# Kernel tuning notes

Measured on AMD Instinct MI355X. Metric: run time of the kernel, lower is better.

The kernel has to match this reference:

```python
import jax, jax.numpy as jnp
import numpy as np
from itertools import product

GRID = 256          # voxels per axis
SCALE = 0.005       # regular grid spacing (transform diagonal)
OFFSET = -0.64      # grid origin (transform translation)
K = 2_000_000       # number of query points


def setup_inputs() -> dict:
    key = jax.random.key(0)
    kx, kv = jax.random.split(key)
    # query points uniform in [-0.6, 0.6]^3 (inside grid domain)
    x = (jax.random.uniform(kx, (K, 3), dtype=jnp.float32) - 0.5) * 1.2
    # SDF voxel grid values
    values = jax.random.normal(kv, (GRID, GRID, GRID), dtype=jnp.float32)
    # regular per-axis grid point coordinates (as in get_grid_pts)
    ax = (jnp.arange(GRID, dtype=jnp.float32) * SCALE + OFFSET)
    return {"x": x, "values": values, "px": ax, "py": ax, "pz": ax}


def _trilinear_interp(pts_xyz, values, axes):
    # pts_xyz: [K,3]; values: [Nx,Ny,Nz]; axes: (px,py,pz) sorted 1D coords
    idxs, dists, overalls = [], [], []
    for d, p in enumerate(axes):
        c = pts_xyz[:, d]                               # [K]
        n = p.shape[0]
        # torch.bucketize(x, p) with right=False == searchsorted side='left'
        ir = jnp.searchsorted(p, c, side="left")
        ir = jnp.minimum(ir, n - 1)
        il = jnp.clip(ir - 1, 0, n - 1)
        dl = jnp.maximum(c - p[il], 0.0)
        dr = jnp.maximum(p[ir] - c, 0.0)
        both_zero = (dl == 0.0) & (dr == 0.0)           # exactly on a grid point
        dl = jnp.where(both_zero, 1.0, dl)
        dr = jnp.where(both_zero, 1.0, dr)
        idxs.append((il, ir))
        dists.append((dl, dr))
        overalls.append(dl + dr)
    numerator = 0.0
    for onoff in product([0, 1], repeat=3):             # 8 corners
        ix, iy, iz = (idx[o] for o, idx in zip(onoff, idxs))
        w = dists[0][1 - onoff[0]] * dists[1][1 - onoff[1]] * dists[2][1 - onoff[2]]
        numerator = numerator + values[ix, iy, iz] * w
    denominator = overalls[0] * overalls[1] * overalls[2]
    return numerator / denominator                      # [K]


def reference(x, values, px, py, pz):
    pts = x.reshape(-1, 3).astype(jnp.float32)
    return _trilinear_interp(pts, values, (px, py, pz))  # squeezed [K]
```

## Files before the change

### kernel.cpp

```cpp
#include <hip/hip_runtime.h>

#define GRIDN 256
#define BPA 8
#define NBINS (BPA * BPA * BPA)
#define CAP 6144
#define CURSOR_STRIDE 16
#define FKEYS 512


__device__ __forceinline__ int cell_guess(float c) {
    float t = (c + 0.64f) * 200.0f;
    int i = (int)t;
    return min(max(i, 0), GRIDN - 1);
}

__device__ __forceinline__ void dim_interp(float c, const float* __restrict__ p,
                                           int& il, int& ir, float& dl, float& dr) {
    const float SCALE = 0.005f;
    const float OFFSET = -0.64f;
    float t = (c - OFFSET) * (1.0f / SCALE);
    int i = (int)ceilf(t);
    i = min(max(i, 0), GRIDN - 1);
    while (i < GRIDN - 1 && p[i] < c) ++i;
    while (i > 0 && p[i - 1] >= c) --i;
    ir = i;
    il = max(i - 1, 0);
    dl = fmaxf(c - p[il], 0.0f);
    dr = fmaxf(p[ir] - c, 0.0f);
    if (dl == 0.0f && dr == 0.0f) { dl = 1.0f; dr = 1.0f; }
}

__device__ __forceinline__ float interp_point_ax(float cx, float cy, float cz,
                                                 const float* __restrict__ values,
                                                 const float* __restrict__ ax,
                                                 const float* __restrict__ ay,
                                                 const float* __restrict__ az) {
    int ixl, ixr, iyl, iyr, izl, izr;
    float dxl, dxr, dyl, dyr, dzl, dzr;
    dim_interp(cx, ax, ixl, ixr, dxl, dxr);
    dim_interp(cy, ay, iyl, iyr, dyl, dyr);
    dim_interp(cz, az, izl, izr, dzl, dzr);
    int bxl = ixl << 16, bxr = ixr << 16;
    int byl = iyl << 8,  byr = iyr << 8;
    float num =
        values[bxl + byl + izl] * (dxr * dyr * dzr) +
        values[bxl + byl + izr] * (dxr * dyr * dzl) +
        values[bxl + byr + izl] * (dxr * dyl * dzr) +
        values[bxl + byr + izr] * (dxr * dyl * dzl) +
        values[bxr + byl + izl] * (dxl * dyr * dzr) +
        values[bxr + byl + izr] * (dxl * dyr * dzl) +
        values[bxr + byr + izl] * (dxl * dyl * dzr) +
        values[bxr + byr + izr] * (dxl * dyl * dzl);
    float den = (dxl + dxr) * (dyl + dyr) * (dzl + dzr);
    return num / den;
}

__device__ __forceinline__ float interp_zpair(float cx, float cy, float cz,
                                              const float* __restrict__ values,
                                              const float* __restrict__ sax) {
    int ixl, ixr, iyl, iyr, izl, izr;
    float dxl, dxr, dyl, dyr, dzl, dzr;
    dim_interp(cx, sax,             ixl, ixr, dxl, dxr);
    dim_interp(cy, sax + GRIDN,     iyl, iyr, dyl, dyr);
    dim_interp(cz, sax + 2 * GRIDN, izl, izr, dzl, dzr);

    int bxl = ixl << 16, bxr = ixr << 16;
    int byl = iyl << 8,  byr = iyr << 8;

    float2 vll, vlr, vrl, vrr;
    __builtin_memcpy(&vll, &values[bxl + byl + izl], 8);
    __builtin_memcpy(&vlr, &values[bxl + byr + izl], 8);
    __builtin_memcpy(&vrl, &values[bxr + byl + izl], 8);
    __builtin_memcpy(&vrr, &values[bxr + byr + izl], 8);

    bool zsame = (izr == izl);
    float zll = vll.x, zlr = zsame ? vll.x : vll.y;
    float yll = vlr.x, ylr = zsame ? vlr.x : vlr.y;
    float xll = vrl.x, xlr = zsame ? vrl.x : vrl.y;
    float wll = vrr.x, wlr = zsame ? vrr.x : vrr.y;

    float num =
        (dxr * dyr) * (zll * dzr + zlr * dzl) +
        (dxr * dyl) * (yll * dzr + ylr * dzl) +
        (dxl * dyr) * (xll * dzr + xlr * dzl) +
        (dxl * dyl) * (wll * dzr + wlr * dzl);
    float den = (dxl + dxr) * (dyl + dyr) * (dzl + dzr);
    return num / den;
}


__global__ void init_cursors(unsigned* __restrict__ cursor) {
    int t = blockIdx.x * blockDim.x + threadIdx.x;
    if (t < NBINS) cursor[t * CURSOR_STRIDE] = (unsigned)(t * CAP);
}


__global__ __launch_bounds__(1024) void bin_scatter2(
        const float* __restrict__ x, int K,
        unsigned* __restrict__ cursor,
        float4* __restrict__ records,
        int* __restrict__ inv,
        const float* __restrict__ values,
        const float* __restrict__ px,
        const float* __restrict__ py,
        const float* __restrict__ pz,
        float* __restrict__ out) {
    __shared__ unsigned cnt[NBINS];
    __shared__ unsigned slotcur[NBINS];

    int base = blockIdx.x * 4096;
    int end = min(base + 4096, K);

    for (int t = threadIdx.x; t < NBINS; t += 1024) cnt[t] = 0;
    __syncthreads();

    for (int i = base + threadIdx.x; i < end; i += 1024) {
        int bx = cell_guess(x[3 * i]) >> 5;
        int by = cell_guess(x[3 * i + 1]) >> 5;
        int bz = cell_guess(x[3 * i + 2]) >> 5;
        atomicAdd(&cnt[(bx * BPA + by) * BPA + bz], 1u);
    }
    __syncthreads();

    for (int t = threadIdx.x; t < NBINS; t += 1024)
        slotcur[t] = cnt[t] ? atomicAdd(&cursor[t * CURSOR_STRIDE], cnt[t]) : 0u;
    __syncthreads();

    for (int i = base + threadIdx.x; i < end; i += 1024) {
        float cx = x[3 * i], cy = x[3 * i + 1], cz = x[3 * i + 2];
        int bx = cell_guess(cx) >> 5;
        int by = cell_guess(cy) >> 5;
        int bz = cell_guess(cz) >> 5;
        int b = (bx * BPA + by) * BPA + bz;
        unsigned s = atomicAdd(&slotcur[b], 1u);
        if (s < (unsigned)((b + 1) * CAP)) {
            records[s] = make_float4(cx, cy, cz, 0.0f);
            inv[i] = (int)s;
        } else {
            inv[i] = -1;
            out[i] = interp_point_ax(cx, cy, cz, values, px, py, pz);
        }
    }
}


#define K2_THREADS 1024

__global__ __launch_bounds__(K2_THREADS) void interp_binsort(
        const float4* __restrict__ records,
        const unsigned* __restrict__ cursor,
        const float* __restrict__ values,
        const float* __restrict__ px,
        const float* __restrict__ py,
        const float* __restrict__ pz,
        float* __restrict__ res) {
    __shared__ float sax[3 * GRIDN];
    __shared__ unsigned hist[FKEYS];
    __shared__ unsigned short skeys[CAP];
    __shared__ unsigned short order[CAP];
    __shared__ float sx[CAP], sy[CAP], sz[CAP];
    __shared__ float sres[CAP];

    int nb = gridDim.x;
    int b = blockIdx.x;
    int q = nb >> 3;
    int bin = (b & 7) * q + (b >> 3);

    for (int t = threadIdx.x; t < GRIDN; t += K2_THREADS) {
        sax[t] = px[t];
        sax[GRIDN + t] = py[t];
        sax[2 * GRIDN + t] = pz[t];
    }
    for (int t = threadIdx.x; t < FKEYS; t += K2_THREADS) hist[t] = 0;
    __syncthreads();

    unsigned binstart = (unsigned)bin * CAP;
    unsigned segend = min(cursor[bin * CURSOR_STRIDE], binstart + CAP);
    int npts = (int)(segend - binstart);
    if (npts <= 0) return;

    int cbx = (bin >> 6) << 5;
    int cby = ((bin >> 3) & 7) << 5;
    int cbz = (bin & 7) << 5;

    for (int pt = threadIdx.x; pt < npts; pt += K2_THREADS) {
        float4 rec = records[binstart + pt];
        sx[pt] = rec.x; sy[pt] = rec.y; sz[pt] = rec.z;
        int fx = (cell_guess(rec.x) - cbx) >> 2;
        int fy = (cell_guess(rec.y) - cby) >> 2;
        int fz = (cell_guess(rec.z) - cbz) >> 2;
        fx = min(max(fx, 0), 7); fy = min(max(fy, 0), 7); fz = min(max(fz, 0), 7);
        int k = ((fx << 3) | fy) << 3 | fz;
        skeys[pt] = (unsigned short)k;
        atomicAdd(&hist[k], 1u);
    }
    __syncthreads();

    unsigned own = (threadIdx.x < FKEYS) ? hist[threadIdx.x] : 0u;
    for (int off = 1; off < FKEYS; off <<= 1) {
        unsigned v = 0;
        if (threadIdx.x < FKEYS && (int)threadIdx.x >= off) v = hist[threadIdx.x - off];
        __syncthreads();
        if (threadIdx.x < FKEYS) hist[threadIdx.x] += v;
        __syncthreads();
    }
    if (threadIdx.x < FKEYS) hist[threadIdx.x] -= own;
    __syncthreads();

    for (int pt = threadIdx.x; pt < npts; pt += K2_THREADS) {
        unsigned slot = atomicAdd(&hist[skeys[pt]], 1u);
        order[slot] = (unsigned short)pt;
    }
    __syncthreads();

    for (int pt = threadIdx.x; pt < npts; pt += K2_THREADS) {
        int j = order[pt];
        sres[j] = interp_zpair(sx[j], sy[j], sz[j], values, sax);
    }
    __syncthreads();

    for (int pt = threadIdx.x; pt < npts; pt += K2_THREADS)
        res[binstart + pt] = sres[pt];
}


__global__ void unscatter(const int* __restrict__ inv,
                          const float* __restrict__ res,
                          float* __restrict__ out, int K) {
    int i = blockIdx.x * blockDim.x + threadIdx.x;
    if (i >= K) return;
    int s = inv[i];
    if (s >= 0) out[i] = res[s];
}


__global__ void trilerp_direct(const float* __restrict__ x,
                               const float* __restrict__ values,
                               const float* __restrict__ px,
                               const float* __restrict__ py,
                               const float* __restrict__ pz,
                               float* __restrict__ out, int K) {
    int i = blockIdx.x * blockDim.x + threadIdx.x;
    if (i >= K) return;
    out[i] = interp_point_ax(x[3 * i], x[3 * i + 1], x[3 * i + 2],
                             values, px, py, pz);
}

extern "C" void kernel_launch(void* const* d_in, const int* in_sizes, int n_in,
                              void* d_out, int out_size, void* d_ws, size_t ws_size,
                              hipStream_t stream) {
    const float* x      = (const float*)d_in[0];
    const float* values = (const float*)d_in[1];
    const float* px     = (const float*)d_in[2];
    const float* py     = (const float*)d_in[3];
    const float* pz     = (const float*)d_in[4];
    float* out = (float*)d_out;

    int K = in_sizes[0] / 3;

    size_t cursor_bytes  = (size_t)NBINS * CURSOR_STRIDE * 4;
    size_t records_bytes = (size_t)NBINS * CAP * 16;
    size_t inv_bytes     = (size_t)K * 4;
    size_t res_bytes     = (size_t)NBINS * CAP * 4;
    size_t need = cursor_bytes + records_bytes + inv_bytes + res_bytes;

    if (ws_size < need) {
        int grid = (K + 255) / 256;
        trilerp_direct<<<grid, 256, 0, stream>>>(x, values, px, py, pz, out, K);
        return;
    }

    char* p = (char*)d_ws;
    unsigned* cursor = (unsigned*)p;  p += cursor_bytes;
    float4* records  = (float4*)p;    p += records_bytes;
    int* inv         = (int*)p;       p += inv_bytes;
    float* res       = (float*)p;

    init_cursors<<<2, 256, 0, stream>>>(cursor);

    int nblk1 = (K + 4095) / 4096;
    bin_scatter2<<<nblk1, 1024, 0, stream>>>(x, K, cursor, records, inv,
                                             values, px, py, pz, out);

    interp_binsort<<<NBINS, K2_THREADS, 0, stream>>>(records, cursor,
                                                     values, px, py, pz, res);

    int nblk3 = (K + 255) / 256;
    unscatter<<<nblk3, 256, 0, stream>>>(inv, res, out, K);
}
```

Before: 85.63 us.

## Use 1024 smaller bins, wave-shuffle histogram scan, and memset cursor init

Splits the grid into 1024 spatial bins, halving the z extent of each, with half the per-bin capacity. This shrinks the per-block shared memory footprint so more interp blocks can be resident and the grid is more evenly loaded. The 512-entry Hillis-Steele histogram scan with many barriers becomes a 256-entry wave-shuffle scan plus a small cross-wave fixup. Cursors are now relative offsets zeroed with a memset instead of an init kernel. More bins raise the chance of overflow into the slow direct fallback path.

```diff
diff --git a/kernel.cpp b/kernel.cpp
--- a/kernel.cpp
+++ b/kernel.cpp
@@ -1,11 +1,10 @@
 #include <hip/hip_runtime.h>
 
 #define GRIDN 256
-#define BPA 8
-#define NBINS (BPA * BPA * BPA)
-#define CAP 6144
+#define NBINS 1024
+#define CAP 3072
 #define CURSOR_STRIDE 16
-#define FKEYS 512
+#define FKEYS 256
 
 
 __device__ __forceinline__ int cell_guess(float c) {
@@ -88,10 +87,8 @@
     return num / den;
 }
 
-
-__global__ void init_cursors(unsigned* __restrict__ cursor) {
-    int t = blockIdx.x * blockDim.x + threadIdx.x;
-    if (t < NBINS) cursor[t * CURSOR_STRIDE] = (unsigned)(t * CAP);
+__device__ __forceinline__ int bin_of_cells(int cgx, int cgy, int cgz) {
+    return ((cgx >> 5) << 7) | ((cgy >> 5) << 4) | (cgz >> 4);
 }
 
 
@@ -115,23 +112,21 @@
     __syncthreads();
 
     for (int i = base + threadIdx.x; i < end; i += 1024) {
-        int bx = cell_guess(x[3 * i]) >> 5;
-        int by = cell_guess(x[3 * i + 1]) >> 5;
-        int bz = cell_guess(x[3 * i + 2]) >> 5;
-        atomicAdd(&cnt[(bx * BPA + by) * BPA + bz], 1u);
+        int b = bin_of_cells(cell_guess(x[3 * i]), cell_guess(x[3 * i + 1]),
+                             cell_guess(x[3 * i + 2]));
+        atomicAdd(&cnt[b], 1u);
     }
     __syncthreads();
 
     for (int t = threadIdx.x; t < NBINS; t += 1024)
-        slotcur[t] = cnt[t] ? atomicAdd(&cursor[t * CURSOR_STRIDE], cnt[t]) : 0u;
+        slotcur[t] = cnt[t] ? ((unsigned)t * CAP +
+                               atomicAdd(&cursor[t * CURSOR_STRIDE], cnt[t]))
+                            : 0u;
     __syncthreads();
 
     for (int i = base + threadIdx.x; i < end; i += 1024) {
         float cx = x[3 * i], cy = x[3 * i + 1], cz = x[3 * i + 2];
-        int bx = cell_guess(cx) >> 5;
-        int by = cell_guess(cy) >> 5;
-        int bz = cell_guess(cz) >> 5;
-        int b = (bx * BPA + by) * BPA + bz;
+        int b = bin_of_cells(cell_guess(cx), cell_guess(cy), cell_guess(cz));
         unsigned s = atomicAdd(&slotcur[b], 1u);
         if (s < (unsigned)((b + 1) * CAP)) {
             records[s] = make_float4(cx, cy, cz, 0.0f);
@@ -156,7 +151,8 @@
         float* __restrict__ res) {
     __shared__ float sax[3 * GRIDN];
     __shared__ unsigned hist[FKEYS];
-    __shared__ unsigned short skeys[CAP];
+    __shared__ unsigned wsum[4];
+    __shared__ unsigned char skeys[CAP];
     __shared__ unsigned short order[CAP];
     __shared__ float sx[CAP], sy[CAP], sz[CAP];
     __shared__ float sres[CAP];
@@ -171,17 +167,16 @@
         sax[GRIDN + t] = py[t];
         sax[2 * GRIDN + t] = pz[t];
     }
-    for (int t = threadIdx.x; t < FKEYS; t += K2_THREADS) hist[t] = 0;
+    if (threadIdx.x < FKEYS) hist[threadIdx.x] = 0;
     __syncthreads();
 
     unsigned binstart = (unsigned)bin * CAP;
-    unsigned segend = min(cursor[bin * CURSOR_STRIDE], binstart + CAP);
-    int npts = (int)(segend - binstart);
+    int npts = min((int)cursor[bin * CURSOR_STRIDE], CAP);
     if (npts <= 0) return;
 
-    int cbx = (bin >> 6) << 5;
-    int cby = ((bin >> 3) & 7) << 5;
-    int cbz = (bin & 7) << 5;
+    int cbx = (bin >> 7) << 5;
+    int cby = ((bin >> 4) & 7) << 5;
+    int cbz = (bin & 15) << 4;
 
     for (int pt = threadIdx.x; pt < npts; pt += K2_THREADS) {
         float4 rec = records[binstart + pt];
@@ -189,22 +184,31 @@
         int fx = (cell_guess(rec.x) - cbx) >> 2;
         int fy = (cell_guess(rec.y) - cby) >> 2;
         int fz = (cell_guess(rec.z) - cbz) >> 2;
-        fx = min(max(fx, 0), 7); fy = min(max(fy, 0), 7); fz = min(max(fz, 0), 7);
-        int k = ((fx << 3) | fy) << 3 | fz;
-        skeys[pt] = (unsigned short)k;
+        fx = min(max(fx, 0), 7); fy = min(max(fy, 0), 7); fz = min(max(fz, 0), 3);
+        int k = (((fx << 3) | fy) << 2) | fz;
+        skeys[pt] = (unsigned char)k;
         atomicAdd(&hist[k], 1u);
     }
     __syncthreads();
 
-    unsigned own = (threadIdx.x < FKEYS) ? hist[threadIdx.x] : 0u;
-    for (int off = 1; off < FKEYS; off <<= 1) {
-        unsigned v = 0;
-        if (threadIdx.x < FKEYS && (int)threadIdx.x >= off) v = hist[threadIdx.x - off];
-        __syncthreads();
-        if (threadIdx.x < FKEYS) hist[threadIdx.x] += v;
-        __syncthreads();
-    }
-    if (threadIdx.x < FKEYS) hist[threadIdx.x] -= own;
+    unsigned v = 0, s = 0;
+    int lane = threadIdx.x & 63, w = threadIdx.x >> 6;
+    if (threadIdx.x < FKEYS) {
+        v = hist[threadIdx.x];
+        s = v;
+        for (int off = 1; off < 64; off <<= 1) {
+            unsigned t = __shfl_up(s, off, 64);
+            if (lane >= off) s += t;
+        }
+        if (lane == 63) wsum[w] = s;
+    }
+    __syncthreads();
+    if (threadIdx.x == 0) {
+        unsigned a = 0;
+        for (int i = 0; i < 4; ++i) { unsigned t = wsum[i]; wsum[i] = a; a += t; }
+    }
+    __syncthreads();
+    if (threadIdx.x < FKEYS) hist[threadIdx.x] = s - v + wsum[w];
     __syncthreads();
 
     for (int pt = threadIdx.x; pt < npts; pt += K2_THREADS) {
@@ -276,7 +280,7 @@
     int* inv         = (int*)p;       p += inv_bytes;
     float* res       = (float*)p;
 
-    init_cursors<<<2, 256, 0, stream>>>(cursor);
+    hipMemsetAsync(cursor, 0, cursor_bytes, stream);
 
     int nblk1 = (K + 4095) / 4096;
     bin_scatter2<<<nblk1, 1024, 0, stream>>>(x, K, cursor, records, inv,
```

Result: slower. 95.22 us (+11.2%).

## Split each spatial bin across two blocks and use wave-shuffle prefix scan

Applied to the files above, without the earlier changes.

The interpolation kernel now launches two blocks per spatial bin, each sorting and interpolating half of the bin's points. This halves per-block shared memory so more blocks can be resident, and it doubles the grid size. The 512-entry histogram prefix sum becomes a warp-shuffle scan plus a small cross-wave fixup, replacing the barrier-heavy Hillis-Steele loop. Cursors now hold relative counts, so they are zeroed with a memset instead of an init kernel. The trade-off is that each half sorts only locally, which may reduce cache locality across the two halves of a bin.

```diff
diff --git a/kernel.cpp b/kernel.cpp
--- a/kernel.cpp
+++ b/kernel.cpp
@@ -4,6 +4,8 @@
 #define BPA 8
 #define NBINS (BPA * BPA * BPA)
 #define CAP 6144
+#define HALF 2
+#define CAPH (CAP / HALF)
 #define CURSOR_STRIDE 16
 #define FKEYS 512
 
@@ -89,12 +91,6 @@
 }
 
 
-__global__ void init_cursors(unsigned* __restrict__ cursor) {
-    int t = blockIdx.x * blockDim.x + threadIdx.x;
-    if (t < NBINS) cursor[t * CURSOR_STRIDE] = (unsigned)(t * CAP);
-}
-
-
 __global__ __launch_bounds__(1024) void bin_scatter2(
         const float* __restrict__ x, int K,
         unsigned* __restrict__ cursor,
@@ -123,7 +119,9 @@
     __syncthreads();
 
     for (int t = threadIdx.x; t < NBINS; t += 1024)
-        slotcur[t] = cnt[t] ? atomicAdd(&cursor[t * CURSOR_STRIDE], cnt[t]) : 0u;
+        slotcur[t] = cnt[t] ? ((unsigned)t * CAP +
+                               atomicAdd(&cursor[t * CURSOR_STRIDE], cnt[t]))
+                            : 0u;
     __syncthreads();
 
     for (int i = base + threadIdx.x; i < end; i += 1024) {
@@ -146,7 +144,7 @@
 
 #define K2_THREADS 1024
 
-__global__ __launch_bounds__(K2_THREADS) void interp_binsort(
+__global__ __launch_bounds__(K2_THREADS) void interp_halfsort(
         const float4* __restrict__ records,
         const unsigned* __restrict__ cursor,
         const float* __restrict__ values,
@@ -156,15 +154,18 @@
         float* __restrict__ res) {
     __shared__ float sax[3 * GRIDN];
     __shared__ unsigned hist[FKEYS];
-    __shared__ unsigned short skeys[CAP];
-    __shared__ unsigned short order[CAP];
-    __shared__ float sx[CAP], sy[CAP], sz[CAP];
-    __shared__ float sres[CAP];
+    __shared__ unsigned wsum[8];
+    __shared__ unsigned short skeys[CAPH];
+    __shared__ unsigned short order[CAPH];
+    __shared__ float sx[CAPH], sy[CAPH], sz[CAPH];
+    __shared__ float sres[CAPH];
 
     int nb = gridDim.x;
     int b = blockIdx.x;
     int q = nb >> 3;
-    int bin = (b & 7) * q + (b >> 3);
+    int lin = (b & 7) * q + (b >> 3);
+    int bin = lin >> 1;
+    int half = lin & 1;
 
     for (int t = threadIdx.x; t < GRIDN; t += K2_THREADS) {
         sax[t] = px[t];
@@ -175,52 +176,66 @@
     __syncthreads();
 
     unsigned binstart = (unsigned)bin * CAP;
-    unsigned segend = min(cursor[bin * CURSOR_STRIDE], binstart + CAP);
-    int npts = (int)(segend - binstart);
+    int npts = min((int)cursor[bin * CURSOR_STRIDE], CAP);
     if (npts <= 0) return;
+
+    int cnt_h = (npts + HALF - 1) / HALF;
+    int lo = half * cnt_h;
+    int n = min(npts, lo + cnt_h) - lo;
+    if (n <= 0) return;
+    unsigned base = binstart + lo;
 
     int cbx = (bin >> 6) << 5;
     int cby = ((bin >> 3) & 7) << 5;
     int cbz = (bin & 7) << 5;
 
-    for (int pt = threadIdx.x; pt < npts; pt += K2_THREADS) {
-        float4 rec = records[binstart + pt];
+    for (int pt = threadIdx.x; pt < n; pt += K2_THREADS) {
+        float4 rec = records[base + pt];
         sx[pt] = rec.x; sy[pt] = rec.y; sz[pt] = rec.z;
         int fx = (cell_guess(rec.x) - cbx) >> 2;
         int fy = (cell_guess(rec.y) - cby) >> 2;
         int fz = (cell_guess(rec.z) - cbz) >> 2;
         fx = min(max(fx, 0), 7); fy = min(max(fy, 0), 7); fz = min(max(fz, 0), 7);
-        int k = ((fx << 3) | fy) << 3 | fz;
+        int k = (((fx << 3) | fy) << 3) | fz;
         skeys[pt] = (unsigned short)k;
         atomicAdd(&hist[k], 1u);
     }
     __syncthreads();
 
-    unsigned own = (threadIdx.x < FKEYS) ? hist[threadIdx.x] : 0u;
-    for (int off = 1; off < FKEYS; off <<= 1) {
-        unsigned v = 0;
-        if (threadIdx.x < FKEYS && (int)threadIdx.x >= off) v = hist[threadIdx.x - off];
-        __syncthreads();
-        if (threadIdx.x < FKEYS) hist[threadIdx.x] += v;
-        __syncthreads();
-    }
-    if (threadIdx.x < FKEYS) hist[threadIdx.x] -= own;
-    __syncthreads();
-
-    for (int pt = threadIdx.x; pt < npts; pt += K2_THREADS) {
+    unsigned v = 0, s = 0;
+    int lane = threadIdx.x & 63, w = threadIdx.x >> 6;
+    if (threadIdx.x < FKEYS) {
+        v = hist[threadIdx.x];
+        s = v;
+        for (int off = 1; off < 64; off <<= 1) {
+            unsigned t = __shfl_up(s, off, 64);
+            if (lane >= off) s += t;
+        }
+        if (lane == 63) wsum[w] = s;
+    }
+    __syncthreads();
+    if (threadIdx.x == 0) {
+        unsigned a = 0;
+        for (int i = 0; i < 8; ++i) { unsigned t = wsum[i]; wsum[i] = a; a += t; }
+    }
+    __syncthreads();
+    if (threadIdx.x < FKEYS) hist[threadIdx.x] = s - v + wsum[w];
+    __syncthreads();
+
+    for (int pt = threadIdx.x; pt < n; pt += K2_THREADS) {
         unsigned slot = atomicAdd(&hist[skeys[pt]], 1u);
         order[slot] = (unsigned short)pt;
     }
     __syncthreads();
 
-    for (int pt = threadIdx.x; pt < npts; pt += K2_THREADS) {
+    for (int pt = threadIdx.x; pt < n; pt += K2_THREADS) {
         int j = order[pt];
         sres[j] = interp_zpair(sx[j], sy[j], sz[j], values, sax);
     }
     __syncthreads();
 
-    for (int pt = threadIdx.x; pt < npts; pt += K2_THREADS)
-        res[binstart + pt] = sres[pt];
+    for (int pt = threadIdx.x; pt < n; pt += K2_THREADS)
+        res[base + pt] = sres[pt];
 }
 
 
@@ -276,14 +291,14 @@
     int* inv         = (int*)p;       p += inv_bytes;
     float* res       = (float*)p;
 
-    init_cursors<<<2, 256, 0, stream>>>(cursor);
+    hipMemsetAsync(cursor, 0, cursor_bytes, stream);
 
     int nblk1 = (K + 4095) / 4096;
     bin_scatter2<<<nblk1, 1024, 0, stream>>>(x, K, cursor, records, inv,
                                              values, px, py, pz, out);
 
-    interp_binsort<<<NBINS, K2_THREADS, 0, stream>>>(records, cursor,
-                                                     values, px, py, pz, res);
+    interp_halfsort<<<NBINS * HALF, K2_THREADS, 0, stream>>>(records, cursor,
+                                                             values, px, py, pz, res);
 
     int nblk3 = (K + 255) / 256;
     unscatter<<<nblk3, 256, 0, stream>>>(inv, res, out, K);
```

Measured after the change: 82.37 us (median of 2 runs). 1.04x faster.

## Stage per-bin voxel region in shared memory instead of locally sorting points

Applied to the files above, without the earlier changes.

The per-bin interpolation kernel no longer sorts points with a shared-memory histogram. It now loads each bin's grid subregion (35x35x24 with a halo, in two z passes) into LDS and gathers the corner values from there, falling back to global gathers for points outside the staged region. Each thread keeps up to six point records in registers. The cursor is now zeroed with hipMemsetAsync and becomes a relative count, with the bin base added in the scatter kernel. This trades random global gathers for bulk coalesced tile loads, but each bin reloads a larger halo'd region and the kernel adds extra barriers.

```diff
diff --git a/kernel.cpp b/kernel.cpp
--- a/kernel.cpp
+++ b/kernel.cpp
@@ -5,7 +5,13 @@
 #define NBINS (BPA * BPA * BPA)
 #define CAP 6144
 #define CURSOR_STRIDE 16
-#define FKEYS 512
+#define RX 35
+#define RY 35
+#define RZ 24
+#define SEGS (RZ / 4)
+#define NROWS (RX * RY)
+#define REGF (NROWS * RZ)
+#define PPT 6
 
 
 __device__ __forceinline__ int cell_guess(float c) {
@@ -55,45 +61,6 @@
     return num / den;
 }
 
-__device__ __forceinline__ float interp_zpair(float cx, float cy, float cz,
-                                              const float* __restrict__ values,
-                                              const float* __restrict__ sax) {
-    int ixl, ixr, iyl, iyr, izl, izr;
-    float dxl, dxr, dyl, dyr, dzl, dzr;
-    dim_interp(cx, sax,             ixl, ixr, dxl, dxr);
-    dim_interp(cy, sax + GRIDN,     iyl, iyr, dyl, dyr);
-    dim_interp(cz, sax + 2 * GRIDN, izl, izr, dzl, dzr);
-
-    int bxl = ixl << 16, bxr = ixr << 16;
-    int byl = iyl << 8,  byr = iyr << 8;
-
-    float2 vll, vlr, vrl, vrr;
-    __builtin_memcpy(&vll, &values[bxl + byl + izl], 8);
-    __builtin_memcpy(&vlr, &values[bxl + byr + izl], 8);
-    __builtin_memcpy(&vrl, &values[bxr + byl + izl], 8);
-    __builtin_memcpy(&vrr, &values[bxr + byr + izl], 8);
-
-    bool zsame = (izr == izl);
-    float zll = vll.x, zlr = zsame ? vll.x : vll.y;
-    float yll = vlr.x, ylr = zsame ? vlr.x : vlr.y;
-    float xll = vrl.x, xlr = zsame ? vrl.x : vrl.y;
-    float wll = vrr.x, wlr = zsame ? vrr.x : vrr.y;
-
-    float num =
-        (dxr * dyr) * (zll * dzr + zlr * dzl) +
-        (dxr * dyl) * (yll * dzr + ylr * dzl) +
-        (dxl * dyr) * (xll * dzr + xlr * dzl) +
-        (dxl * dyl) * (wll * dzr + wlr * dzl);
-    float den = (dxl + dxr) * (dyl + dyr) * (dzl + dzr);
-    return num / den;
-}
-
-
-__global__ void init_cursors(unsigned* __restrict__ cursor) {
-    int t = blockIdx.x * blockDim.x + threadIdx.x;
-    if (t < NBINS) cursor[t * CURSOR_STRIDE] = (unsigned)(t * CAP);
-}
-
 
 __global__ __launch_bounds__(1024) void bin_scatter2(
         const float* __restrict__ x, int K,
@@ -123,7 +90,9 @@
     __syncthreads();
 
     for (int t = threadIdx.x; t < NBINS; t += 1024)
-        slotcur[t] = cnt[t] ? atomicAdd(&cursor[t * CURSOR_STRIDE], cnt[t]) : 0u;
+        slotcur[t] = cnt[t] ? ((unsigned)t * CAP +
+                               atomicAdd(&cursor[t * CURSOR_STRIDE], cnt[t]))
+                            : 0u;
     __syncthreads();
 
     for (int i = base + threadIdx.x; i < end; i += 1024) {
@@ -144,9 +113,7 @@
 }
 
 
-#define K2_THREADS 1024
-
-__global__ __launch_bounds__(K2_THREADS) void interp_binsort(
+__global__ __launch_bounds__(1024) void interp_staged(
         const float4* __restrict__ records,
         const unsigned* __restrict__ cursor,
         const float* __restrict__ values,
@@ -155,72 +122,87 @@
         const float* __restrict__ pz,
         float* __restrict__ res) {
     __shared__ float sax[3 * GRIDN];
-    __shared__ unsigned hist[FKEYS];
-    __shared__ unsigned short skeys[CAP];
-    __shared__ unsigned short order[CAP];
-    __shared__ float sx[CAP], sy[CAP], sz[CAP];
-    __shared__ float sres[CAP];
+    __shared__ float reg[REGF];
 
     int nb = gridDim.x;
     int b = blockIdx.x;
     int q = nb >> 3;
     int bin = (b & 7) * q + (b >> 3);
 
-    for (int t = threadIdx.x; t < GRIDN; t += K2_THREADS) {
+    for (int t = threadIdx.x; t < GRIDN; t += 1024) {
         sax[t] = px[t];
         sax[GRIDN + t] = py[t];
         sax[2 * GRIDN + t] = pz[t];
     }
-    for (int t = threadIdx.x; t < FKEYS; t += K2_THREADS) hist[t] = 0;
-    __syncthreads();
 
     unsigned binstart = (unsigned)bin * CAP;
-    unsigned segend = min(cursor[bin * CURSOR_STRIDE], binstart + CAP);
-    int npts = (int)(segend - binstart);
-    if (npts <= 0) return;
+    int n = min((int)cursor[bin * CURSOR_STRIDE], CAP);
 
     int cbx = (bin >> 6) << 5;
     int cby = ((bin >> 3) & 7) << 5;
     int cbz = (bin & 7) << 5;
-
-    for (int pt = threadIdx.x; pt < npts; pt += K2_THREADS) {
-        float4 rec = records[binstart + pt];
-        sx[pt] = rec.x; sy[pt] = rec.y; sz[pt] = rec.z;
-        int fx = (cell_guess(rec.x) - cbx) >> 2;
-        int fy = (cell_guess(rec.y) - cby) >> 2;
-        int fz = (cell_guess(rec.z) - cbz) >> 2;
-        fx = min(max(fx, 0), 7); fy = min(max(fy, 0), 7); fz = min(max(fz, 0), 7);
-        int k = ((fx << 3) | fy) << 3 | fz;
-        skeys[pt] = (unsigned short)k;
-        atomicAdd(&hist[k], 1u);
-    }
-    __syncthreads();
-
-    unsigned own = (threadIdx.x < FKEYS) ? hist[threadIdx.x] : 0u;
-    for (int off = 1; off < FKEYS; off <<= 1) {
-        unsigned v = 0;
-        if (threadIdx.x < FKEYS && (int)threadIdx.x >= off) v = hist[threadIdx.x - off];
+    int rx0 = cbx - 2, ry0 = cby - 2;
+
+    float4 r[PPT];
+    #pragma unroll
+    for (int k = 0; k < PPT; ++k) {
+        int idx = (int)threadIdx.x + k * 1024;
+        r[k] = (idx < n) ? records[binstart + idx] : make_float4(0.f, 0.f, 0.f, 0.f);
+    }
+
+    for (int pass = 0; pass < 2; ++pass) {
         __syncthreads();
-        if (threadIdx.x < FKEYS) hist[threadIdx.x] += v;
+        int z0 = cbz - 4 + pass * 16;
+
+        for (int l = threadIdx.x; l < NROWS * SEGS; l += 1024) {
+            int row = l / SEGS;
+            int seg = l - row * SEGS;
+            int u = row / RY;
+            int v = row - u * RY;
+            int gx = min(max(rx0 + u, 0), GRIDN - 1);
+            int gy = min(max(ry0 + v, 0), GRIDN - 1);
+            int gz = min(max(z0 + seg * 4, 0), GRIDN - 4);
+            float4 val = *reinterpret_cast<const float4*>(
+                &values[(gx << 16) | (gy << 8) | gz]);
+            *reinterpret_cast<float4*>(&reg[row * RZ + seg * 4]) = val;
+        }
         __syncthreads();
-    }
-    if (threadIdx.x < FKEYS) hist[threadIdx.x] -= own;
-    __syncthreads();
-
-    for (int pt = threadIdx.x; pt < npts; pt += K2_THREADS) {
-        unsigned slot = atomicAdd(&hist[skeys[pt]], 1u);
-        order[slot] = (unsigned short)pt;
-    }
-    __syncthreads();
-
-    for (int pt = threadIdx.x; pt < npts; pt += K2_THREADS) {
-        int j = order[pt];
-        sres[j] = interp_zpair(sx[j], sy[j], sz[j], values, sax);
-    }
-    __syncthreads();
-
-    for (int pt = threadIdx.x; pt < npts; pt += K2_THREADS)
-        res[binstart + pt] = sres[pt];
+
+        #pragma unroll
+        for (int k = 0; k < PPT; ++k) {
+            int idx = (int)threadIdx.x + k * 1024;
+            if (idx >= n) continue;
+            float4 rc = r[k];
+            if (((cell_guess(rc.z) - cbz) >> 4) != pass) continue;
+
+            int ixl, ixr, iyl, iyr, izl, izr;
+            float dxl, dxr, dyl, dyr, dzl, dzr;
+            dim_interp(rc.x, sax,             ixl, ixr, dxl, dxr);
+            dim_interp(rc.y, sax + GRIDN,     iyl, iyr, dyl, dyr);
+            dim_interp(rc.z, sax + 2 * GRIDN, izl, izr, dzl, dzr);
+
+            int lx = ixl - rx0, ly = iyl - ry0, lz = izl - z0;
+            float outv;
+            if ((unsigned)lx < RX - 1 && (unsigned)ly < RY - 1 &&
+                (unsigned)lz < RZ - 1 &&
+                ixr == ixl + 1 && iyr == iyl + 1 && izr == izl + 1) {
+                const float* p00 = &reg[(lx * RY + ly) * RZ + lz];
+                const float* p01 = &reg[(lx * RY + (ly + 1)) * RZ + lz];
+                const float* p10 = &reg[((lx + 1) * RY + ly) * RZ + lz];
+                const float* p11 = &reg[((lx + 1) * RY + (ly + 1)) * RZ + lz];
+                float num =
+                    (dxr * dyr) * (p00[0] * dzr + p00[1] * dzl) +
+                    (dxr * dyl) * (p01[0] * dzr + p01[1] * dzl) +
+                    (dxl * dyr) * (p10[0] * dzr + p10[1] * dzl) +
+                    (dxl * dyl) * (p11[0] * dzr + p11[1] * dzl);
+                float den = (dxl + dxr) * (dyl + dyr) * (dzl + dzr);
+                outv = num / den;
+            } else {
+                outv = interp_point_ax(rc.x, rc.y, rc.z, values, px, py, pz);
+            }
+            res[binstart + idx] = outv;
+        }
+    }
 }
 
 
@@ -276,14 +258,14 @@
     int* inv         = (int*)p;       p += inv_bytes;
     float* res       = (float*)p;
 
-    init_cursors<<<2, 256, 0, stream>>>(cursor);
+    hipMemsetAsync(cursor, 0, cursor_bytes, stream);
 
     int nblk1 = (K + 4095) / 4096;
     bin_scatter2<<<nblk1, 1024, 0, stream>>>(x, K, cursor, records, inv,
                                              values, px, py, pz, out);
 
-    interp_binsort<<<NBINS, K2_THREADS, 0, stream>>>(records, cursor,
-                                                     values, px, py, pz, res);
+    interp_staged<<<NBINS, 1024, 0, stream>>>(records, cursor,
+                                              values, px, py, pz, res);
 
     int nblk3 = (K + 255) / 256;
     unscatter<<<nblk3, 256, 0, stream>>>(inv, res, out, K);
```

Measured after the change: 103.4 us. 20.7% more time.
